# Kernel optimization log

Measured on AMD Instinct MI355X. Metric: run time of the kernel, lower is better.

## Reference

```python
import jax, jax.numpy as jnp
import numpy as np

N_NODES = 100000
N_EDGES = 1600000
D = 128
NEG_SLOPE = 0.01  # torch F.leaky_relu default


def setup_inputs() -> dict:
    key = jax.random.key(0)
    k1, k2, k3, k4, k5 = jax.random.split(key, 5)
    nfeat = jax.random.normal(k1, (N_NODES, D), dtype=jnp.float32)
    edge_src = jax.random.randint(k2, (N_EDGES,), 0, N_NODES, dtype=jnp.int32)
    edge_dst = jax.random.randint(k3, (N_EDGES,), 0, N_NODES, dtype=jnp.int32)
    edge_w = jax.random.uniform(k4, (N_EDGES,), dtype=jnp.float32)
    W = jax.random.normal(k5, (D, D), dtype=jnp.float32) * (1.0 / np.sqrt(D))
    return {"nfeat": nfeat, "edge_src": edge_src, "edge_dst": edge_dst,
            "edge_w": edge_w, "W": W}


def reference(nfeat, edge_src, edge_dst, edge_w, W):
    # message: m_e = h[src_e] * w_e  (u_mul_e)
    msg = nfeat[edge_src] * edge_w[:, None]          # [E, D]
    # reduce: h_neighbor[v] = sum_{e: dst(e)=v} m_e  (fn.sum)
    h_neighbor = jax.ops.segment_sum(msg, edge_dst, num_segments=nfeat.shape[0])  # [N, D]
    # Bi-interaction residual: leaky_relu(Linear(h * h_neighbor)); dropout = identity (eval)
    out = jax.nn.leaky_relu((nfeat * h_neighbor) @ W.T, negative_slope=NEG_SLOPE)
    return out
```

## Files before the change

### kernel.cpp

```cpp
#include <hip/hip_runtime.h>
#include <hip/hip_fp16.h>

#define NNODES 100000
#define NEDGES 1600000
#define DIM    128
#define NEG_SLOPE 0.01f
#define NB_SCAN ((NNODES + 1023) / 1024)
#define NPART 8
#define PART_SZ ((NNODES + NPART - 1) / NPART)
#define PCAP 220000
#define PCUR_STRIDE 32
#define CHUNK 2048
#define GEMM_TILES ((NNODES + 63) / 64)

typedef _Float16     v8h __attribute__((ext_vector_type(8)));
typedef float        v4f __attribute__((ext_vector_type(4)));
typedef int          v4i __attribute__((ext_vector_type(4)));
typedef int          v2i __attribute__((ext_vector_type(2)));
typedef float        v4x __attribute__((ext_vector_type(4)));
typedef unsigned int v2u __attribute__((ext_vector_type(2)));
typedef unsigned int v4u __attribute__((ext_vector_type(4)));

static inline size_t align256(size_t x) { return (x + 255) & ~(size_t)255; }

union HU { unsigned int u; __half2 h; };

__global__ __launch_bounds__(256) void zero_f32(float* __restrict__ p, int n4) {
    int i = blockIdx.x * blockDim.x + threadIdx.x;
    int stride = gridDim.x * blockDim.x;
    float4 z = make_float4(0.f, 0.f, 0.f, 0.f);
    for (; i < n4; i += stride) ((float4*)p)[i] = z;
}

__global__ __launch_bounds__(256) void prep(const float* __restrict__ nf,
                                            const float* __restrict__ W,
                                            __half* __restrict__ nf16,
                                            __half* __restrict__ W16,
                                            int* __restrict__ counts,
                                            int* __restrict__ pcur) {
    int i = blockIdx.x * 256 + threadIdx.x;
    int stride = gridDim.x * 256;
    for (int j = i; j < NNODES * DIM / 4; j += stride) {
        v4x v = __builtin_nontemporal_load((const v4x*)nf + j);
        HU a, b;
        a.h = __float22half2_rn(make_float2(v.x, v.y));
        b.h = __float22half2_rn(make_float2(v.z, v.w));
        ((uint2*)nf16)[j] = make_uint2(a.u, b.u);
    }
    const float4* Wg4 = (const float4*)W;
    for (int j = i; j < DIM * DIM / 8; j += stride) {
        float4 lo = Wg4[j * 2], hi = Wg4[j * 2 + 1];
        HU a, b, c, d;
        a.h = __float22half2_rn(make_float2(lo.x, lo.y));
        b.h = __float22half2_rn(make_float2(lo.z, lo.w));
        c.h = __float22half2_rn(make_float2(hi.x, hi.y));
        d.h = __float22half2_rn(make_float2(hi.z, hi.w));
        ((uint4*)W16)[j] = make_uint4(a.u, b.u, c.u, d.u);
    }
    v4i z = (v4i){0, 0, 0, 0};
    for (int j = i; j < NNODES / 4; j += stride)
        *((v4i*)counts + j) = z;
    if (i < NPART * PCUR_STRIDE) pcur[i] = 0;
}

__global__ __launch_bounds__(256) void split_edges(const int* __restrict__ esrc,
                                                   const int* __restrict__ edst,
                                                   const float* __restrict__ ew,
                                                   int* __restrict__ pcur,
                                                   int2* __restrict__ pairs) {
    __shared__ int wtot[4][NPART];
    __shared__ int wbase[4][NPART];
    __shared__ int gbase[NPART];
    int tid = threadIdx.x;
    int wave = tid >> 6, lane = tid & 63;
    unsigned long long lt = (1ull << lane) - 1ull;

    int nq = NEDGES / 4;
    int qA = (blockIdx.x * CHUNK >> 2) + tid;
    int qB = qA + 256;

    v4i dA = (v4i){0,0,0,0}, sA = (v4i){0,0,0,0};
    v4x wA = (v4x){0,0,0,0};
    v4i dB = (v4i){0,0,0,0}, sB = (v4i){0,0,0,0};
    v4x wB = (v4x){0,0,0,0};
    bool vA = qA < nq, vB = qB < nq;
    if (vA) {
        dA = __builtin_nontemporal_load((const v4i*)edst + qA);
        sA = __builtin_nontemporal_load((const v4i*)esrc + qA);
        wA = __builtin_nontemporal_load((const v4x*)ew + qA);
    }
    if (vB) {
        dB = __builtin_nontemporal_load((const v4i*)edst + qB);
        sB = __builtin_nontemporal_load((const v4i*)esrc + qB);
        wB = __builtin_nontemporal_load((const v4x*)ew + qB);
    }

    int prt[8]; int rnk[8]; int2 pv[8];
    #pragma unroll
    for (int k = 0; k < 4; ++k) {
        int d = dA[k], s = sA[k];
        int p = vA ? (int)((unsigned)d / PART_SZ) : -1;
        prt[k] = p;
        pv[k] = make_int2(((d - p * PART_SZ) << 17) | s, __float_as_int(wA[k]));
        int d2 = dB[k], s2 = sB[k];
        int p2 = vB ? (int)((unsigned)d2 / PART_SZ) : -1;
        prt[k + 4] = p2;
        pv[k + 4] = make_int2(((d2 - p2 * PART_SZ) << 17) | s2, __float_as_int(wB[k]));
    }

    int runcnt = 0;
    #pragma unroll
    for (int s = 0; s < 8; ++s) {
        int myp = prt[s];
        unsigned long long mymask = 0;
        int addc = 0;
        #pragma unroll
        for (int p = 0; p < NPART; ++p) {
            unsigned long long m = __ballot(myp == p);
            if (myp == p) mymask = m;
            if (lane == p) addc = (int)__popcll(m);
        }
        int wr = __shfl(runcnt, myp < 0 ? 0 : myp);
        rnk[s] = wr + (int)__popcll(mymask & lt);
        runcnt += addc;
    }

    if (lane < NPART) wtot[wave][lane] = runcnt;
    __syncthreads();
    if (tid < NPART) {
        int t0 = wtot[0][tid], t1 = wtot[1][tid], t2 = wtot[2][tid], t3 = wtot[3][tid];
        wbase[0][tid] = 0; wbase[1][tid] = t0;
        wbase[2][tid] = t0 + t1; wbase[3][tid] = t0 + t1 + t2;
        gbase[tid] = atomicAdd(&pcur[tid * PCUR_STRIDE], t0 + t1 + t2 + t3);
    }
    __syncthreads();

    #pragma unroll
    for (int s = 0; s < 8; ++s) {
        int p = prt[s];
        if (p >= 0) {
            int slot = gbase[p] + wbase[wave][p] + rnk[s];
            if (slot < PCAP)
                pairs[(size_t)p * PCAP + slot] = pv[s];
        }
    }
}

__global__ __launch_bounds__(256) void hist_part(const int2* __restrict__ pairs,
                                                 const int* __restrict__ pcur,
                                                 int* __restrict__ counts) {
    int part = blockIdx.x & (NPART - 1);
    int n = pcur[part * PCUR_STRIDE];
    if (n > PCAP) n = PCAP;
    const int2* base = pairs + (size_t)part * PCAP;
    int cbase = part * PART_SZ;
    int t = (blockIdx.x >> 3) * 256 + threadIdx.x;
    int stride = (gridDim.x >> 3) * 256;
    int nh = n >> 1;
    for (int i = t; i < nh; i += stride) {
        v4i pr = __builtin_nontemporal_load((const v4i*)base + i);
        atomicAdd(&counts[cbase + ((unsigned)pr.x >> 17)], 1);
        atomicAdd(&counts[cbase + ((unsigned)pr.z >> 17)], 1);
    }
    if ((blockIdx.x >> 3) == 0 && threadIdx.x == 0 && (n & 1)) {
        int2 pr = base[n - 1];
        atomicAdd(&counts[cbase + ((unsigned)pr.x >> 17)], 1);
    }
}

__global__ __launch_bounds__(256) void scan1(const int* __restrict__ counts,
                                             int* __restrict__ offsets,
                                             int* __restrict__ blocksum) {
    __shared__ int lds[256];
    int tid = threadIdx.x;
    int base = blockIdx.x * 1024 + tid * 4;
    int c0 = (base + 0 < NNODES) ? counts[base + 0] : 0;
    int c1 = (base + 1 < NNODES) ? counts[base + 1] : 0;
    int c2 = (base + 2 < NNODES) ? counts[base + 2] : 0;
    int c3 = (base + 3 < NNODES) ? counts[base + 3] : 0;
    int t = c0 + c1 + c2 + c3;
    lds[tid] = t;
    __syncthreads();
    for (int d = 1; d < 256; d <<= 1) {
        int v = lds[tid];
        int add = (tid >= d) ? lds[tid - d] : 0;
        __syncthreads();
        lds[tid] = v + add;
        __syncthreads();
    }
    int incl = lds[tid];
    int excl = incl - t;
    if (base + 0 < NNODES) offsets[base + 0] = excl;
    if (base + 1 < NNODES) offsets[base + 1] = excl + c0;
    if (base + 2 < NNODES) offsets[base + 2] = excl + c0 + c1;
    if (base + 3 < NNODES) offsets[base + 3] = excl + c0 + c1 + c2;
    if (tid == 255) blocksum[blockIdx.x] = incl;
}

__global__ __launch_bounds__(128) void scan2p(int* __restrict__ blocksum, int nb) {
    __shared__ int lds[128];
    int tid = threadIdx.x;
    int v = (tid < nb) ? blocksum[tid] : 0;
    lds[tid] = v;
    __syncthreads();
    for (int d = 1; d < 128; d <<= 1) {
        int x = lds[tid];
        int add = (tid >= d) ? lds[tid - d] : 0;
        __syncthreads();
        lds[tid] = x + add;
        __syncthreads();
    }
    if (tid < nb) blocksum[tid] = lds[tid] - v;
}

__global__ __launch_bounds__(256) void scan3(int* __restrict__ offsets,
                                             const int* __restrict__ blocksum) {
    int add = blocksum[blockIdx.x];
    int base = blockIdx.x * 1024 + threadIdx.x * 4;
    #pragma unroll
    for (int i = 0; i < 4; ++i) {
        int idx = base + i;
        if (idx < NNODES) offsets[idx] += add;
    }
}

__global__ __launch_bounds__(256) void fill_part2(const int2* __restrict__ pairs,
                                                  const int* __restrict__ pcur,
                                                  int* __restrict__ offsets,
                                                  int2* __restrict__ bins) {
    int part = blockIdx.x & (NPART - 1);
    int n = pcur[part * PCUR_STRIDE];
    if (n > PCAP) n = PCAP;
    const int2* base = pairs + (size_t)part * PCAP;
    int cbase = part * PART_SZ;
    int t = (blockIdx.x >> 3) * 256 + threadIdx.x;
    int stride = (gridDim.x >> 3) * 256;
    int nh = n >> 1;
    for (int i = t; i < nh; i += stride) {
        v4i pr = __builtin_nontemporal_load((const v4i*)base + i);
        int d0 = cbase + ((unsigned)pr.x >> 17);
        int p0 = atomicAdd(&offsets[d0], 1);
        bins[p0] = make_int2(pr.x & 0x1FFFF, pr.y);
        int d1 = cbase + ((unsigned)pr.z >> 17);
        int p1 = atomicAdd(&offsets[d1], 1);
        bins[p1] = make_int2(pr.z & 0x1FFFF, pr.w);
    }
    if ((blockIdx.x >> 3) == 0 && threadIdx.x == 0 && (n & 1)) {
        int2 pr = base[n - 1];
        int d = cbase + ((unsigned)pr.x >> 17);
        int p = atomicAdd(&offsets[d], 1);
        bins[p] = make_int2(pr.x & 0x1FFFF, pr.y);
    }
}

__global__ __launch_bounds__(256) void pull_x16(const __half* __restrict__ nf16,
                                                const int* __restrict__ offsets,
                                                const int* __restrict__ counts,
                                                const int2* __restrict__ bins,
                                                __half* __restrict__ x16) {
    int gid = blockIdx.x * 256 + threadIdx.x;
    int v = gid >> 5;
    int lane = gid & 31;
    if (v >= NNODES) return;
    int end = offsets[v];
    int start = end - counts[v];
    const uint2* nf2 = (const uint2*)nf16;
    float4 a0 = make_float4(0.f, 0.f, 0.f, 0.f);
    float4 a1 = make_float4(0.f, 0.f, 0.f, 0.f);
    float4 a2 = make_float4(0.f, 0.f, 0.f, 0.f);
    float4 a3 = make_float4(0.f, 0.f, 0.f, 0.f);
    int k = start;
    for (; k + 4 <= end; k += 4) {
        v2i e0 = __builtin_nontemporal_load((const v2i*)bins + k);
        v2i e1 = __builtin_nontemporal_load((const v2i*)bins + k + 1);
        v2i e2 = __builtin_nontemporal_load((const v2i*)bins + k + 2);
        v2i e3 = __builtin_nontemporal_load((const v2i*)bins + k + 3);
        uint2 u0 = nf2[(size_t)e0.x * 32 + lane];
        uint2 u1 = nf2[(size_t)e1.x * 32 + lane];
        uint2 u2 = nf2[(size_t)e2.x * 32 + lane];
        uint2 u3 = nf2[(size_t)e3.x * 32 + lane];
        float w0 = __int_as_float(e0.y), w1 = __int_as_float(e1.y);
        float w2 = __int_as_float(e2.y), w3 = __int_as_float(e3.y);
        HU h; float2 f;
        h.u = u0.x; f = __half22float2(h.h); a0.x += w0 * f.x; a0.y += w0 * f.y;
        h.u = u0.y; f = __half22float2(h.h); a0.z += w0 * f.x; a0.w += w0 * f.y;
        h.u = u1.x; f = __half22float2(h.h); a1.x += w1 * f.x; a1.y += w1 * f.y;
        h.u = u1.y; f = __half22float2(h.h); a1.z += w1 * f.x; a1.w += w1 * f.y;
        h.u = u2.x; f = __half22float2(h.h); a2.x += w2 * f.x; a2.y += w2 * f.y;
        h.u = u2.y; f = __half22float2(h.h); a2.z += w2 * f.x; a2.w += w2 * f.y;
        h.u = u3.x; f = __half22float2(h.h); a3.x += w3 * f.x; a3.y += w3 * f.y;
        h.u = u3.y; f = __half22float2(h.h); a3.z += w3 * f.x; a3.w += w3 * f.y;
    }
    for (; k < end; ++k) {
        v2i e = __builtin_nontemporal_load((const v2i*)bins + k);
        float w = __int_as_float(e.y);
        uint2 u = nf2[(size_t)e.x * 32 + lane];
        HU h; float2 f;
        h.u = u.x; f = __half22float2(h.h); a0.x += w * f.x; a0.y += w * f.y;
        h.u = u.y; f = __half22float2(h.h); a0.z += w * f.x; a0.w += w * f.y;
    }
    float4 acc;
    acc.x = (a0.x + a1.x) + (a2.x + a3.x);
    acc.y = (a0.y + a1.y) + (a2.y + a3.y);
    acc.z = (a0.z + a1.z) + (a2.z + a3.z);
    acc.w = (a0.w + a1.w) + (a2.w + a3.w);
    uint2 un = nf2[(size_t)v * 32 + lane];
    HU h; float2 f;
    h.u = un.x; f = __half22float2(h.h); acc.x *= f.x; acc.y *= f.y;
    h.u = un.y; f = __half22float2(h.h); acc.z *= f.x; acc.w *= f.y;
    HU o0, o1;
    o0.h = __float22half2_rn(make_float2(acc.x, acc.y));
    o1.h = __float22half2_rn(make_float2(acc.z, acc.w));
    v2u ov = (v2u){o0.u, o1.u};
    __builtin_nontemporal_store(ov, (v2u*)x16 + (size_t)v * 32 + lane);
}

__global__ __launch_bounds__(256) void gemm16(const __half* __restrict__ x16,
                                              const __half* __restrict__ W16,
                                              float* __restrict__ out) {
    __shared__ _Float16 Wl[128 * 128];
    __shared__ _Float16 Xl[64 * 128];
    int tid = threadIdx.x;

    const v4u* Wg = (const v4u*)W16;
    for (int i = tid; i < 2048; i += 256) {
        int r = i >> 4, c = i & 15;
        v4u u = Wg[i];
        *(v4u*)&Wl[r * 128 + ((c ^ (r & 7)) << 3)] = u;
    }

    int rbase = blockIdx.x * 64;
    for (int i = tid; i < 1024; i += 256) {
        int r = i >> 4, c = i & 15;
        int grow = rbase + r;
        v4u u = (v4u){0u, 0u, 0u, 0u};
        if (grow < NNODES)
            u = __builtin_nontemporal_load((const v4u*)x16 + (size_t)grow * 16 + c);
        *(v4u*)&Xl[r * 128 + ((c ^ (r & 7)) << 3)] = u;
    }
    __syncthreads();

    int wave = tid >> 6;
    int lane = tid & 63;
    int n = lane & 15;
    int g = lane >> 4;

    v4f acc[8];
    #pragma unroll
    for (int jb = 0; jb < 8; ++jb) acc[jb] = (v4f){0.f, 0.f, 0.f, 0.f};

    #pragma unroll
    for (int kb = 0; kb < 4; ++kb) {
        v8h a = *(v8h*)&Xl[(wave * 16 + n) * 128 + (((kb * 4 + g) ^ (n & 7)) << 3)];
        #pragma unroll
        for (int jb = 0; jb < 8; ++jb) {
            v8h b = *(v8h*)&Wl[(jb * 16 + n) * 128 + (((kb * 4 + g) ^ (n & 7)) << 3)];
            acc[jb] = __builtin_amdgcn_mfma_f32_16x16x32_f16(a, b, acc[jb], 0, 0, 0);
        }
    }

    int row0 = rbase + wave * 16 + g * 4;
    #pragma unroll
    for (int jb = 0; jb < 8; ++jb) {
        #pragma unroll
        for (int reg = 0; reg < 4; ++reg) {
            int r = row0 + reg;
            if (r < NNODES) {
                float v = acc[jb][reg];
                v = v >= 0.f ? v : NEG_SLOPE * v;
                __builtin_nontemporal_store(v, out + (size_t)r * 128 + jb * 16 + n);
            }
        }
    }
}

__global__ __launch_bounds__(256) void hist_dst4(const int* __restrict__ edst,
                                                 int* __restrict__ counts) {
    int i = blockIdx.x * 256 + threadIdx.x;
    if (i < NEDGES / 4) {
        int4 d = ((const int4*)edst)[i];
        atomicAdd(&counts[d.x], 1);
        atomicAdd(&counts[d.y], 1);
        atomicAdd(&counts[d.z], 1);
        atomicAdd(&counts[d.w], 1);
    }
}

__global__ __launch_bounds__(256) void fill_part(const int* __restrict__ esrc,
                                                 const int* __restrict__ edst,
                                                 const float* __restrict__ ew,
                                                 int* __restrict__ offsets,
                                                 int2* __restrict__ bins) {
    int part = blockIdx.x & (NPART - 1);
    int lo = part * PART_SZ;
    int hi = lo + PART_SZ;
    int t = (blockIdx.x >> 3) * 256 + threadIdx.x;
    int stride = (gridDim.x >> 3) * 256;
    int nq = NEDGES / 4;
    for (int i = t; i < nq; i += stride) {
        int4 d = ((const int4*)edst)[i];
        int e = i * 4;
        if (d.x >= lo && d.x < hi) {
            int p = atomicAdd(&offsets[d.x], 1);
            bins[p] = make_int2(esrc[e + 0], __float_as_int(ew[e + 0]));
        }
        if (d.y >= lo && d.y < hi) {
            int p = atomicAdd(&offsets[d.y], 1);
            bins[p] = make_int2(esrc[e + 1], __float_as_int(ew[e + 1]));
        }
        if (d.z >= lo && d.z < hi) {
            int p = atomicAdd(&offsets[d.z], 1);
            bins[p] = make_int2(esrc[e + 2], __float_as_int(ew[e + 2]));
        }
        if (d.w >= lo && d.w < hi) {
            int p = atomicAdd(&offsets[d.w], 1);
            bins[p] = make_int2(esrc[e + 3], __float_as_int(ew[e + 3]));
        }
    }
}

__global__ __launch_bounds__(256) void scatter_edges(
    const float* __restrict__ nfeat, const int* __restrict__ esrc,
    const int* __restrict__ edst, const float* __restrict__ ew,
    float* __restrict__ hn) {
    long long t = (long long)blockIdx.x * 256 + threadIdx.x;
    int e = (int)(t >> 5);
    if (e >= NEDGES) return;
    int lane = (int)(t & 31);
    int s = esrc[e];
    int d = edst[e];
    float w = ew[e];
    float4 v = ((const float4*)(nfeat + (size_t)s * DIM))[lane];
    float* o = hn + (size_t)d * DIM + lane * 4;
    unsafeAtomicAdd(o + 0, v.x * w);
    unsafeAtomicAdd(o + 1, v.y * w);
    unsafeAtomicAdd(o + 2, v.z * w);
    unsafeAtomicAdd(o + 3, v.w * w);
}

__global__ __launch_bounds__(256) void elem_mul(const float* __restrict__ nfeat,
                                                float* __restrict__ hn, int n4) {
    int i = blockIdx.x * blockDim.x + threadIdx.x;
    int stride = gridDim.x * blockDim.x;
    for (; i < n4; i += stride) {
        float4 a = ((const float4*)nfeat)[i];
        float4 b = ((float4*)hn)[i];
        b.x *= a.x; b.y *= a.y; b.z *= a.z; b.w *= a.w;
        ((float4*)hn)[i] = b;
    }
}

__global__ __launch_bounds__(256) void bi_gemm2(
    const float* __restrict__ x, const float* __restrict__ W,
    float* __restrict__ out) {
    extern __shared__ float lds[];
    float4* W4  = (float4*)lds;
    float*  xs  = lds + 128 * 128;
    float4* xs4 = (float4*)xs;
    int tid = threadIdx.x;
    const float4* Wg = (const float4*)W;
    for (int i = tid; i < 128 * 32; i += 256) {
        int j = i >> 5, d4 = i & 31;
        W4[(j << 5) | (d4 ^ ((j >> 2) & 7))] = Wg[i];
    }
    __syncthreads();
    int tx = tid & 31, ty = tid >> 5;
    int j0 = tx << 2, r0 = ty << 2;
    int ntiles = NNODES / 32;
    for (int tile = blockIdx.x; tile < ntiles; tile += gridDim.x) {
        int rbase = tile * 32;
        for (int i = tid; i < 32 * 32; i += 256)
            xs4[i] = ((const float4*)x)[(size_t)rbase * 32 + i];
        __syncthreads();
        float acc[4][4];
        #pragma unroll
        for (int r = 0; r < 4; ++r)
            #pragma unroll
            for (int j = 0; j < 4; ++j) acc[r][j] = 0.f;
        #pragma unroll 4
        for (int d4 = 0; d4 < 32; ++d4) {
            float4 xv[4], wv[4];
            #pragma unroll
            for (int r = 0; r < 4; ++r) xv[r] = xs4[((r0 + r) << 5) | d4];
            #pragma unroll
            for (int j = 0; j < 4; ++j) {
                int jj = j0 + j;
                wv[j] = W4[(jj << 5) | (d4 ^ ((jj >> 2) & 7))];
            }
            #pragma unroll
            for (int r = 0; r < 4; ++r)
                #pragma unroll
                for (int j = 0; j < 4; ++j) {
                    acc[r][j] += xv[r].x * wv[j].x;
                    acc[r][j] += xv[r].y * wv[j].y;
                    acc[r][j] += xv[r].z * wv[j].z;
                    acc[r][j] += xv[r].w * wv[j].w;
                }
        }
        __syncthreads();
        #pragma unroll
        for (int r = 0; r < 4; ++r) {
            float4 o;
            o.x = acc[r][0] >= 0.f ? acc[r][0] : NEG_SLOPE * acc[r][0];
            o.y = acc[r][1] >= 0.f ? acc[r][1] : NEG_SLOPE * acc[r][1];
            o.z = acc[r][2] >= 0.f ? acc[r][2] : NEG_SLOPE * acc[r][2];
            o.w = acc[r][3] >= 0.f ? acc[r][3] : NEG_SLOPE * acc[r][3];
            size_t row = (size_t)(rbase + r0 + r);
            ((float4*)out)[row * (DIM / 4) + tx] = o;
        }
    }
}

extern "C" void kernel_launch(void* const* d_in, const int* in_sizes, int n_in,
                              void* d_out, int out_size, void* d_ws, size_t ws_size,
                              hipStream_t stream) {
    const float* nfeat = (const float*)d_in[0];
    const int*   esrc  = (const int*)d_in[1];
    const int*   edst  = (const int*)d_in[2];
    const float* ew    = (const float*)d_in[3];
    const float* W     = (const float*)d_in[4];
    float* out = (float*)d_out;

    size_t off = 0;
    size_t nf16_off = off;     off += align256((size_t)NNODES * DIM * 2);
    size_t x16_off = off;      off += align256((size_t)NNODES * DIM * 2);
    size_t w16_off = off;      off += align256((size_t)DIM * DIM * 2);
    size_t cnt_off = off;      off += align256((size_t)NNODES * 4);
    size_t ofs_off = off;      off += align256((size_t)NNODES * 4);
    size_t pcur_off = off;     off += align256((size_t)NPART * PCUR_STRIDE * 4);
    size_t bsum_off = off;     off += align256((size_t)NB_SCAN * 4);
    size_t bins_off = off;     off += align256((size_t)NEDGES * 8);
    size_t need_mid = off;
    size_t pair_off = off;     off += align256((size_t)NPART * PCAP * 8);
    size_t need_full = off;

    char* ws = (char*)d_ws;

    if (ws_size >= need_mid) {
        __half* nf16 = (__half*)(ws + nf16_off);
        __half* x16  = (__half*)(ws + x16_off);
        __half* W16  = (__half*)(ws + w16_off);
        int* counts = (int*)(ws + cnt_off);
        int* offsets = (int*)(ws + ofs_off);
        int* pcur = (int*)(ws + pcur_off);
        int* blocksum = (int*)(ws + bsum_off);
        int2* bins = (int2*)(ws + bins_off);
        int2* pairs = (int2*)(ws + pair_off);

        prep<<<2048, 256, 0, stream>>>(nfeat, W, nf16, W16, counts, pcur);
        if (ws_size >= need_full) {
            int sgrid = (NEDGES + CHUNK - 1) / CHUNK;
            split_edges<<<sgrid, 256, 0, stream>>>(esrc, edst, ew, pcur, pairs);
            hist_part<<<2048, 256, 0, stream>>>(pairs, pcur, counts);
            scan1<<<NB_SCAN, 256, 0, stream>>>(counts, offsets, blocksum);
            scan2p<<<1, 128, 0, stream>>>(blocksum, NB_SCAN);
            scan3<<<NB_SCAN, 256, 0, stream>>>(offsets, blocksum);
            fill_part2<<<2048, 256, 0, stream>>>(pairs, pcur, offsets, bins);
        } else {
            int e4grid = (NEDGES / 4 + 255) / 256;
            hist_dst4<<<e4grid, 256, 0, stream>>>(edst, counts);
            scan1<<<NB_SCAN, 256, 0, stream>>>(counts, offsets, blocksum);
            scan2p<<<1, 128, 0, stream>>>(blocksum, NB_SCAN);
            scan3<<<NB_SCAN, 256, 0, stream>>>(offsets, blocksum);
            fill_part<<<2048, 256, 0, stream>>>(esrc, edst, ew, offsets, bins);
        }
        int pgrid = (NNODES * 32 + 255) / 256;
        pull_x16<<<pgrid, 256, 0, stream>>>(nf16, offsets, counts, bins, x16);
        gemm16<<<GEMM_TILES, 256, 0, stream>>>(x16, W16, out);
    } else {
        float* hn = (float*)ws;
        hipFuncSetAttribute((const void*)bi_gemm2,
                            hipFuncAttributeMaxDynamicSharedMemorySize, 81920);
        zero_f32<<<2048, 256, 0, stream>>>(hn, NNODES * DIM / 4);
        int sgrid = (NEDGES * 32 + 255) / 256;
        scatter_edges<<<sgrid, 256, 0, stream>>>(nfeat, esrc, edst, ew, hn);
        elem_mul<<<2048, 256, 0, stream>>>(nfeat, hn, NNODES * DIM / 4);
        bi_gemm2<<<512, 256, 81920, stream>>>(hn, W, out);
    }
}
```

Baseline: 273.7 us.

## Split edges into 64 sub-partitions with LDS atomic ranking

```diff
diff --git a/kernel.cpp b/kernel.cpp
--- a/kernel.cpp
+++ b/kernel.cpp
@@ -8,8 +8,10 @@
 #define NB_SCAN ((NNODES + 1023) / 1024)
 #define NPART 8
 #define PART_SZ ((NNODES + NPART - 1) / NPART)
-#define PCAP 220000
-#define PCUR_STRIDE 32
+#define NSUB 64
+#define SUB_SZ ((NNODES + NSUB - 1) / NSUB)
+#define SCAP 27000
+#define SCUR_STRIDE 32
 #define CHUNK 2048
 #define GEMM_TILES ((NNODES + 63) / 64)
 
@@ -37,7 +39,7 @@
                                             __half* __restrict__ nf16,
                                             __half* __restrict__ W16,
                                             int* __restrict__ counts,
-                                            int* __restrict__ pcur) {
+                                            int* __restrict__ scur) {
     int i = blockIdx.x * 256 + threadIdx.x;
     int stride = gridDim.x * 256;
     for (int j = i; j < NNODES * DIM / 4; j += stride) {
@@ -60,23 +62,24 @@
     v4i z = (v4i){0, 0, 0, 0};
     for (int j = i; j < NNODES / 4; j += stride)
         *((v4i*)counts + j) = z;
-    if (i < NPART * PCUR_STRIDE) pcur[i] = 0;
+    if (i < NSUB * SCUR_STRIDE) scur[i] = 0;
 }
 
 __global__ __launch_bounds__(256) void split_edges(const int* __restrict__ esrc,
                                                    const int* __restrict__ edst,
                                                    const float* __restrict__ ew,
-                                                   int* __restrict__ pcur,
+                                                   int* __restrict__ scur,
                                                    int2* __restrict__ pairs) {
-    __shared__ int wtot[4][NPART];
-    __shared__ int wbase[4][NPART];
-    __shared__ int gbase[NPART];
+    __shared__ int wcnt[4][NSUB];
+    __shared__ int wbase[4][NSUB];
+    __shared__ int gbase[NSUB];
     int tid = threadIdx.x;
-    int wave = tid >> 6, lane = tid & 63;
-    unsigned long long lt = (1ull << lane) - 1ull;
+    int wave = tid >> 6;
+    ((int*)wcnt)[tid] = 0;
+    __syncthreads();
 
     int nq = NEDGES / 4;
-    int qA = (blockIdx.x * CHUNK >> 2) + tid;
+    int qA = blockIdx.x * (CHUNK / 4) + tid;
     int qB = qA + 256;
 
     v4i dA = (v4i){0,0,0,0}, sA = (v4i){0,0,0,0};
@@ -95,76 +98,69 @@
         wB = __builtin_nontemporal_load((const v4x*)ew + qB);
     }
 
-    int prt[8]; int rnk[8]; int2 pv[8];
+    int sp8[8]; int rnk[8]; int2 pv[8];
     #pragma unroll
     for (int k = 0; k < 4; ++k) {
         int d = dA[k], s = sA[k];
-        int p = vA ? (int)((unsigned)d / PART_SZ) : -1;
-        prt[k] = p;
-        pv[k] = make_int2(((d - p * PART_SZ) << 17) | s, __float_as_int(wA[k]));
+        int p = vA ? (int)((unsigned)d / SUB_SZ) : -1;
+        sp8[k] = p;
+        pv[k] = make_int2(((d - p * SUB_SZ) << 17) | s, __float_as_int(wA[k]));
         int d2 = dB[k], s2 = sB[k];
-        int p2 = vB ? (int)((unsigned)d2 / PART_SZ) : -1;
-        prt[k + 4] = p2;
-        pv[k + 4] = make_int2(((d2 - p2 * PART_SZ) << 17) | s2, __float_as_int(wB[k]));
-    }
-
-    int runcnt = 0;
+        int p2 = vB ? (int)((unsigned)d2 / SUB_SZ) : -1;
+        sp8[k + 4] = p2;
+        pv[k + 4] = make_int2(((d2 - p2 * SUB_SZ) << 17) | s2, __float_as_int(wB[k]));
+    }
+
     #pragma unroll
     for (int s = 0; s < 8; ++s) {
-        int myp = prt[s];
-        unsigned long long mymask = 0;
-        int addc = 0;
-        #pragma unroll
-        for (int p = 0; p < NPART; ++p) {
-            unsigned long long m = __ballot(myp == p);
-            if (myp == p) mymask = m;
-            if (lane == p) addc = (int)__popcll(m);
-        }
-        int wr = __shfl(runcnt, myp < 0 ? 0 : myp);
-        rnk[s] = wr + (int)__popcll(mymask & lt);
-        runcnt += addc;
-    }
-
-    if (lane < NPART) wtot[wave][lane] = runcnt;
-    __syncthreads();
-    if (tid < NPART) {
-        int t0 = wtot[0][tid], t1 = wtot[1][tid], t2 = wtot[2][tid], t3 = wtot[3][tid];
+        if (sp8[s] >= 0)
+            rnk[s] = atomicAdd(&wcnt[wave][sp8[s]], 1);
+    }
+    __syncthreads();
+    if (tid < NSUB) {
+        int t0 = wcnt[0][tid], t1 = wcnt[1][tid], t2 = wcnt[2][tid], t3 = wcnt[3][tid];
         wbase[0][tid] = 0; wbase[1][tid] = t0;
         wbase[2][tid] = t0 + t1; wbase[3][tid] = t0 + t1 + t2;
-        gbase[tid] = atomicAdd(&pcur[tid * PCUR_STRIDE], t0 + t1 + t2 + t3);
+        gbase[tid] = atomicAdd(&scur[tid * SCUR_STRIDE], t0 + t1 + t2 + t3);
     }
     __syncthreads();
 
     #pragma unroll
     for (int s = 0; s < 8; ++s) {
-        int p = prt[s];
+        int p = sp8[s];
         if (p >= 0) {
             int slot = gbase[p] + wbase[wave][p] + rnk[s];
-            if (slot < PCAP)
-                pairs[(size_t)p * PCAP + slot] = pv[s];
+            if (slot < SCAP)
+                pairs[(size_t)p * SCAP + slot] = pv[s];
         }
     }
 }
 
 __global__ __launch_bounds__(256) void hist_part(const int2* __restrict__ pairs,
-                                                 const int* __restrict__ pcur,
+                                                 const int* __restrict__ scur,
                                                  int* __restrict__ counts) {
-    int part = blockIdx.x & (NPART - 1);
-    int n = pcur[part * PCUR_STRIDE];
-    if (n > PCAP) n = PCAP;
-    const int2* base = pairs + (size_t)part * PCAP;
-    int cbase = part * PART_SZ;
-    int t = (blockIdx.x >> 3) * 256 + threadIdx.x;
-    int stride = (gridDim.x >> 3) * 256;
-    int nh = n >> 1;
-    for (int i = t; i < nh; i += stride) {
-        v4i pr = __builtin_nontemporal_load((const v4i*)base + i);
-        atomicAdd(&counts[cbase + ((unsigned)pr.x >> 17)], 1);
-        atomicAdd(&counts[cbase + ((unsigned)pr.z >> 17)], 1);
-    }
-    if ((blockIdx.x >> 3) == 0 && threadIdx.x == 0 && (n & 1)) {
-        int2 pr = base[n - 1];
-        atomicAdd(&counts[cbase + ((unsigned)pr.x >> 17)], 1);
+    int b = blockIdx.x;
+    int sp = b & 63;
+    int w = b >> 6;
+    int n = scur[sp * SCUR_STRIDE];
+    if (n > SCAP) n = SCAP;
+    const int2* base = pairs + (size_t)sp * SCAP;
+    int cbase = sp * SUB_SZ;
+    int ng = n >> 2;
+    for (int i = w * 256 + threadIdx.x; i < ng; i += 8192) {
+        v4i a = __builtin_nontemporal_load((const v4i*)base + 2 * i);
+        v4i c = __builtin_nontemporal_load((const v4i*)base + 2 * i + 1);
+        atomicAdd(&counts[cbase + ((unsigned)a.x >> 17)], 1);
+        atomicAdd(&counts[cbase + ((unsigned)a.z >> 17)], 1);
+        atomicAdd(&counts[cbase + ((unsigned)c.x >> 17)], 1);
+        atomicAdd(&counts[cbase + ((unsigned)c.z >> 17)], 1);
+    }
+    if (w == 0 && threadIdx.x < 3) {
+        int idx = (ng << 2) + threadIdx.x;
+        if (idx < n) {
+            int2 pr = base[idx];
+            atomicAdd(&counts[cbase + ((unsigned)pr.x >> 17)], 1);
+        }
     }
 }
 
@@ -225,31 +221,41 @@
 }
 
 __global__ __launch_bounds__(256) void fill_part2(const int2* __restrict__ pairs,
-                                                  const int* __restrict__ pcur,
+                                                  const int* __restrict__ scur,
                                                   int* __restrict__ offsets,
                                                   int2* __restrict__ bins) {
-    int part = blockIdx.x & (NPART - 1);
-    int n = pcur[part * PCUR_STRIDE];
-    if (n > PCAP) n = PCAP;
-    const int2* base = pairs + (size_t)part * PCAP;
-    int cbase = part * PART_SZ;
-    int t = (blockIdx.x >> 3) * 256 + threadIdx.x;
-    int stride = (gridDim.x >> 3) * 256;
-    int nh = n >> 1;
-    for (int i = t; i < nh; i += stride) {
-        v4i pr = __builtin_nontemporal_load((const v4i*)base + i);
-        int d0 = cbase + ((unsigned)pr.x >> 17);
+    int b = blockIdx.x;
+    int sp = b & 63;
+    int w = b >> 6;
+    int n = scur[sp * SCUR_STRIDE];
+    if (n > SCAP) n = SCAP;
+    const int2* base = pairs + (size_t)sp * SCAP;
+    int cbase = sp * SUB_SZ;
+    int ng = n >> 2;
+    for (int i = w * 256 + threadIdx.x; i < ng; i += 8192) {
+        v4i a = __builtin_nontemporal_load((const v4i*)base + 2 * i);
+        v4i c = __builtin_nontemporal_load((const v4i*)base + 2 * i + 1);
+        int d0 = cbase + ((unsigned)a.x >> 17);
         int p0 = atomicAdd(&offsets[d0], 1);
-        bins[p0] = make_int2(pr.x & 0x1FFFF, pr.y);
-        int d1 = cbase + ((unsigned)pr.z >> 17);
+        bins[p0] = make_int2(a.x & 0x1FFFF, a.y);
+        int d1 = cbase + ((unsigned)a.z >> 17);
         int p1 = atomicAdd(&offsets[d1], 1);
-        bins[p1] = make_int2(pr.z & 0x1FFFF, pr.w);
-    }
-    if ((blockIdx.x >> 3) == 0 && threadIdx.x == 0 && (n & 1)) {
-        int2 pr = base[n - 1];
-        int d = cbase + ((unsigned)pr.x >> 17);
-        int p = atomicAdd(&offsets[d], 1);
-        bins[p] = make_int2(pr.x & 0x1FFFF, pr.y);
+        bins[p1] = make_int2(a.z & 0x1FFFF, a.w);
+        int d2 = cbase + ((unsigned)c.x >> 17);
+        int p2 = atomicAdd(&offsets[d2], 1);
+        bins[p2] = make_int2(c.x & 0x1FFFF, c.y);
+        int d3 = cbase + ((unsigned)c.z >> 17);
+        int p3 = atomicAdd(&offsets[d3], 1);
+        bins[p3] = make_int2(c.z & 0x1FFFF, c.w);
+    }
+    if (w == 0 && threadIdx.x < 3) {
+        int idx = (ng << 2) + threadIdx.x;
+        if (idx < n) {
+            int2 pr = base[idx];
+            int d = cbase + ((unsigned)pr.x >> 17);
+            int p = atomicAdd(&offsets[d], 1);
+            bins[p] = make_int2(pr.x & 0x1FFFF, pr.y);
+        }
     }
 }
 
@@ -527,11 +533,11 @@
     size_t w16_off = off;      off += align256((size_t)DIM * DIM * 2);
     size_t cnt_off = off;      off += align256((size_t)NNODES * 4);
     size_t ofs_off = off;      off += align256((size_t)NNODES * 4);
-    size_t pcur_off = off;     off += align256((size_t)NPART * PCUR_STRIDE * 4);
+    size_t scur_off = off;     off += align256((size_t)NSUB * SCUR_STRIDE * 4);
     size_t bsum_off = off;     off += align256((size_t)NB_SCAN * 4);
     size_t bins_off = off;     off += align256((size_t)NEDGES * 8);
     size_t need_mid = off;
-    size_t pair_off = off;     off += align256((size_t)NPART * PCAP * 8);
+    size_t pair_off = off;     off += align256((size_t)NSUB * SCAP * 8);
     size_t need_full = off;
 
     char* ws = (char*)d_ws;
@@ -542,20 +548,20 @@
         __half* W16  = (__half*)(ws + w16_off);
         int* counts = (int*)(ws + cnt_off);
         int* offsets = (int*)(ws + ofs_off);
-        int* pcur = (int*)(ws + pcur_off);
+        int* scur = (int*)(ws + scur_off);
         int* blocksum = (int*)(ws + bsum_off);
         int2* bins = (int2*)(ws + bins_off);
         int2* pairs = (int2*)(ws + pair_off);
 
-        prep<<<2048, 256, 0, stream>>>(nfeat, W, nf16, W16, counts, pcur);
+        prep<<<2048, 256, 0, stream>>>(nfeat, W, nf16, W16, counts, scur);
         if (ws_size >= need_full) {
             int sgrid = (NEDGES + CHUNK - 1) / CHUNK;
-            split_edges<<<sgrid, 256, 0, stream>>>(esrc, edst, ew, pcur, pairs);
-            hist_part<<<2048, 256, 0, stream>>>(pairs, pcur, counts);
+            split_edges<<<sgrid, 256, 0, stream>>>(esrc, edst, ew, scur, pairs);
+            hist_part<<<2048, 256, 0, stream>>>(pairs, scur, counts);
             scan1<<<NB_SCAN, 256, 0, stream>>>(counts, offsets, blocksum);
             scan2p<<<1, 128, 0, stream>>>(blocksum, NB_SCAN);
             scan3<<<NB_SCAN, 256, 0, stream>>>(offsets, blocksum);
-            fill_part2<<<2048, 256, 0, stream>>>(pairs, pcur, offsets, bins);
+            fill_part2<<<2048, 256, 0, stream>>>(pairs, scur, offsets, bins);
         } else {
             int e4grid = (NEDGES / 4 + 255) / 256;
             hist_dst4<<<e4grid, 256, 0, stream>>>(edst, counts);
```

After: 251.0 us. 8.3% less time.
